# Kernel tuning notes

Hardware: AMD Instinct MI355X
Metric: run time of the kernel (lower is better)

Reference implementation:

```python
import jax, jax.numpy as jnp
import numpy as np

IN_DIM = 256
HID = 512
PAT = 10
B = 512
BN_EPS = 1e-5


def setup_inputs() -> dict:
    key = jax.random.key(0)
    ks = jax.random.split(key, 16)
    s = 0.05
    return {
        "x": jax.random.normal(ks[0], (B, IN_DIM), jnp.float32),
        # pattern_detector params
        "W1": jax.random.normal(ks[1], (HID, IN_DIM), jnp.float32) * s,
        "b1": jax.random.normal(ks[2], (HID,), jnp.float32) * s,
        "bn_gamma": 1.0 + jax.random.normal(ks[3], (HID,), jnp.float32) * s,
        "bn_beta": jax.random.normal(ks[4], (HID,), jnp.float32) * s,
        "bn_mean": jax.random.normal(ks[5], (HID,), jnp.float32) * s,
        "bn_var": jnp.ones((HID,), jnp.float32),
        "W2": jax.random.normal(ks[6], (HID // 2, HID), jnp.float32) * s,
        "b2": jax.random.normal(ks[7], (HID // 2,), jnp.float32) * s,
        "W3": jax.random.normal(ks[8], (PAT, HID // 2), jnp.float32) * s,
        "b3": jax.random.normal(ks[9], (PAT,), jnp.float32) * s,
        # similarity_layer params; first Linear weight [HID, 2*IN_DIM] split into
        # the half acting on x_i (Ws1_a) and the half acting on x_j (Ws1_b)
        "Ws1_a": jax.random.normal(ks[10], (HID, IN_DIM), jnp.float32) * s,
        "Ws1_b": jax.random.normal(ks[11], (HID, IN_DIM), jnp.float32) * s,
        "bs1": jax.random.normal(ks[12], (HID,), jnp.float32) * s,
        "ws2": jax.random.normal(ks[13], (HID,), jnp.float32) * s,
        "bs2": jax.random.normal(ks[14], (), jnp.float32) * s,
    }


def reference(x, W1, b1, bn_gamma, bn_beta, bn_mean, bn_var, W2, b2, W3, b3,
              Ws1_a, Ws1_b, bs1, ws2, bs2):
    # --- pattern_detector MLP (eval mode: BN uses running stats, dropout off) ---
    h = x @ W1.T + b1                                    # [B, HID]
    h = bn_gamma * (h - bn_mean) * jax.lax.rsqrt(bn_var + BN_EPS) + bn_beta
    h = jax.nn.relu(h)
    h2 = jax.nn.relu(h @ W2.T + b2)                      # [B, HID//2]
    pattern_scores = h2 @ W3.T + b3                      # [B, PAT]
    pattern_probs = jax.nn.softmax(pattern_scores, axis=-1)

    # --- pairwise similarity: sim(i,j) = MLP(concat(x_i, x_j)) ---
    # Linear([x_i; x_j]) = x_i @ Ws1_a^T + x_j @ Ws1_b^T + bs1, so precompute
    # the two GEMMs and broadcast-add instead of materializing [B,B,2*IN_DIM].
    A = x @ Ws1_a.T                                      # [B, HID]
    C = x @ Ws1_b.T                                      # [B, HID]
    hid = jax.nn.relu(A[:, None, :] + C[None, :, :] + bs1)  # [B, B, HID]
    logits = hid @ ws2 + bs2                             # [B, B]
    sim_full = jax.nn.sigmoid(logits)
    # Original loops i<j only and mirrors, diagonal stays 0. Results are
    # detached (.item()) in torch, so stop_gradient for faithfulness.
    iu = jnp.triu(jnp.ones((x.shape[0], x.shape[0]), sim_full.dtype), k=1)
    S = sim_full * iu
    similarities = jax.lax.stop_gradient(S + S.T)

    return pattern_probs, pattern_scores, similarities
```

## Files before the change

kernel.cpp:

```cpp
#include <hip/hip_runtime.h>
#include <math.h>

#define BN_EPS 1e-5f

typedef _Float16 half2v __attribute__((ext_vector_type(2)));
typedef _Float16 half4v __attribute__((ext_vector_type(4)));
typedef _Float16 half8v __attribute__((ext_vector_type(8)));
typedef __fp16 fp16x8 __attribute__((ext_vector_type(8)));
typedef float floatx4 __attribute__((ext_vector_type(4)));

__device__ __forceinline__ float fdot2(half2v a, half2v b, float c) {
    return __builtin_amdgcn_fdot2(a, b, c, false);
}
__device__ __forceinline__ half2v cvt2(float a, float b) {
    return __builtin_bit_cast(half2v, __builtin_amdgcn_cvt_pkrtz(a, b));
}
__device__ __forceinline__ floatx4 mfma16(half8v a, half8v b, floatx4 c) {
    return __builtin_amdgcn_mfma_f32_16x16x32_f16(
        __builtin_bit_cast(fp16x8, a), __builtin_bit_cast(fp16x8, b), c, 0, 0, 0);
}

__global__ __launch_bounds__(256) void fused3_mfma(
    const float* __restrict__ x,
    const float* __restrict__ W1, const float* __restrict__ b1,
    const float* __restrict__ g, const float* __restrict__ be,
    const float* __restrict__ mu, const float* __restrict__ va,
    const float* __restrict__ Wa, const float* __restrict__ bs1,
    const float* __restrict__ Wb,
    _Float16* __restrict__ h16, _Float16* __restrict__ A16,
    _Float16* __restrict__ C16)
{
    __shared__ _Float16 Xs[64][264];
    __shared__ _Float16 Ws[32][264];

    const int t  = threadIdx.x;
    const int n0 = blockIdx.x * 32;
    const int m0 = blockIdx.y * 64;
    const int z  = blockIdx.z;
    const float* __restrict__ Wp = (z == 0) ? W1 : (z == 1 ? Wa : Wb);

    #pragma unroll
    for (int i = 0; i < 16; ++i) {
        const int cidx = t + i * 256;
        const int row = cidx >> 6;
        const int c4  = cidx & 63;
        const float4 v = *(const float4*)&x[(m0 + row) * 256 + c4 * 4];
        *(half2v*)&Xs[row][c4 * 4 + 0] = cvt2(v.x, v.y);
        *(half2v*)&Xs[row][c4 * 4 + 2] = cvt2(v.z, v.w);
    }
    #pragma unroll
    for (int i = 0; i < 8; ++i) {
        const int cidx = t + i * 256;
        const int row = cidx >> 6;
        const int c4  = cidx & 63;
        const float4 v = *(const float4*)&Wp[(n0 + row) * 256 + c4 * 4];
        *(half2v*)&Ws[row][c4 * 4 + 0] = cvt2(v.x, v.y);
        *(half2v*)&Ws[row][c4 * 4 + 2] = cvt2(v.z, v.w);
    }
    __syncthreads();

    const int wave = t >> 6;
    const int lane = t & 63;
    const int wy = wave >> 1, wx = wave & 1;
    const int lrow = lane & 15;
    const int quad = lane >> 4;
    const int kq = quad * 8;

    floatx4 acc[2] = {{0.f, 0.f, 0.f, 0.f}, {0.f, 0.f, 0.f, 0.f}};

    #pragma unroll
    for (int kc = 0; kc < 256; kc += 32) {
        const half8v a0 = *(const half8v*)&Xs[wy * 32 + lrow][kc + kq];
        const half8v a1 = *(const half8v*)&Xs[wy * 32 + 16 + lrow][kc + kq];
        const half8v b0 = *(const half8v*)&Ws[wx * 16 + lrow][kc + kq];
        acc[0] = mfma16(a0, b0, acc[0]);
        acc[1] = mfma16(a1, b0, acc[1]);
    }

    const int n = n0 + wx * 16 + lrow;
    float scale, off;
    if (z == 0) {
        const float s = g[n] * rsqrtf(va[n] + BN_EPS);
        scale = s;
        off = (b1[n] - mu[n]) * s + be[n];
    } else if (z == 1) {
        scale = 1.f;
        off = bs1[n];
    } else {
        scale = 1.f;
        off = 0.f;
    }
    _Float16* __restrict__ dst = (z == 0) ? h16 : (z == 1 ? A16 : C16);
    #pragma unroll
    for (int mi = 0; mi < 2; ++mi) {
        #pragma unroll
        for (int r = 0; r < 4; ++r) {
            const int m = m0 + wy * 32 + mi * 16 + quad * 4 + r;
            float v = acc[mi][r] * scale + off;
            if (z == 0) v = fmaxf(v, 0.f);
            dst[m * 512 + n] = (_Float16)v;
        }
    }
}

__global__ __launch_bounds__(512) void gemm_h2_kernel(
    const _Float16* __restrict__ h16, const float* __restrict__ W2,
    const float* __restrict__ b2, float* __restrict__ h2o)
{
    __shared__ half2v As16[2][16][36];
    __shared__ half2v Bs16[2][16][72];
    __shared__ float Ps[32][68];

    const int t  = threadIdx.x;
    const int gk = t >> 8;
    const int tl = t & 255;
    const int m0 = blockIdx.y * 32;
    const int n0 = blockIdx.x * 64;
    const int tx = tl & 15, ty = tl >> 4;
    const int kb = gk << 8;

    float acc[2][4] = {};

    for (int kc = 0; kc < 256; kc += 32) {
        const int kk = kb + kc;
        if (tl < 128) {
            const int arow = tl >> 2;
            const int ak8  = (tl & 3) << 3;
            const float4 av = *(const float4*)&h16[(m0 + arow) * 512 + kk + ak8];
            const half2v* ap = (const half2v*)&av;
            const int k2 = ak8 >> 1;
            As16[gk][k2 + 0][arow] = ap[0];
            As16[gk][k2 + 1][arow] = ap[1];
            As16[gk][k2 + 2][arow] = ap[2];
            As16[gk][k2 + 3][arow] = ap[3];
        }
        {
            const int brow = tl >> 2;
            const int bk8  = (tl & 3) << 3;
            const float4 bv0 = *(const float4*)&W2[(n0 + brow) * 512 + kk + bk8];
            const float4 bv1 = *(const float4*)&W2[(n0 + brow) * 512 + kk + bk8 + 4];
            const int k2 = bk8 >> 1;
            Bs16[gk][k2 + 0][brow] = cvt2(bv0.x, bv0.y);
            Bs16[gk][k2 + 1][brow] = cvt2(bv0.z, bv0.w);
            Bs16[gk][k2 + 2][brow] = cvt2(bv1.x, bv1.y);
            Bs16[gk][k2 + 3][brow] = cvt2(bv1.z, bv1.w);
        }
        __syncthreads();

        #pragma unroll
        for (int k2 = 0; k2 < 16; ++k2) {
            const half4v a4 = *(const half4v*)&As16[gk][k2][ty * 2];
            const half8v b8 = *(const half8v*)&Bs16[gk][k2][tx * 4];
            const half2v a0 = __builtin_shufflevector(a4, a4, 0, 1);
            const half2v a1 = __builtin_shufflevector(a4, a4, 2, 3);
            const half2v b0 = __builtin_shufflevector(b8, b8, 0, 1);
            const half2v b1h = __builtin_shufflevector(b8, b8, 2, 3);
            const half2v b2h = __builtin_shufflevector(b8, b8, 4, 5);
            const half2v b3h = __builtin_shufflevector(b8, b8, 6, 7);
            acc[0][0] = fdot2(a0, b0, acc[0][0]);
            acc[0][1] = fdot2(a0, b1h, acc[0][1]);
            acc[0][2] = fdot2(a0, b2h, acc[0][2]);
            acc[0][3] = fdot2(a0, b3h, acc[0][3]);
            acc[1][0] = fdot2(a1, b0, acc[1][0]);
            acc[1][1] = fdot2(a1, b1h, acc[1][1]);
            acc[1][2] = fdot2(a1, b2h, acc[1][2]);
            acc[1][3] = fdot2(a1, b3h, acc[1][3]);
        }
        __syncthreads();
    }

    if (gk == 1) {
        #pragma unroll
        for (int i = 0; i < 2; ++i)
            #pragma unroll
            for (int j = 0; j < 4; ++j)
                Ps[ty * 2 + i][tx * 4 + j] = acc[i][j];
    }
    __syncthreads();
    if (gk == 0) {
        const int n = n0 + tx * 4;
        #pragma unroll
        for (int i = 0; i < 2; ++i) {
            const int m = m0 + ty * 2 + i;
            float4 o;
            o.x = fmaxf(acc[i][0] + Ps[ty * 2 + i][tx * 4 + 0] + b2[n + 0], 0.f);
            o.y = fmaxf(acc[i][1] + Ps[ty * 2 + i][tx * 4 + 1] + b2[n + 1], 0.f);
            o.z = fmaxf(acc[i][2] + Ps[ty * 2 + i][tx * 4 + 2] + b2[n + 2], 0.f);
            o.w = fmaxf(acc[i][3] + Ps[ty * 2 + i][tx * 4 + 3] + b2[n + 3], 0.f);
            *(float4*)&h2o[m * 256 + n] = o;
        }
    }
}

#define SIMS 260
__global__ __launch_bounds__(512) void tail_kernel(
    const float* __restrict__ h2, const float* __restrict__ W3,
    const float* __restrict__ b3,
    const _Float16* __restrict__ A16, const _Float16* __restrict__ C16,
    const float* __restrict__ ws2, const float* __restrict__ bs2,
    float* __restrict__ out)
{
    __shared__ _Float16 Rs[2][32][SIMS];
    __shared__ _Float16 Qs[2][32][SIMS];
    __shared__ half2v wsh[256];
    __shared__ float Ps[32][33];
    __shared__ float Tt[32][33];

    const int bid = blockIdx.x;
    const int t   = threadIdx.x;

    if (bid >= 256) {
        const int lane = t & 63;
        const int r = (bid - 256) * 8 + (t >> 6);

        float p[10];
        #pragma unroll
        for (int q = 0; q < 10; ++q) p[q] = 0.f;
        #pragma unroll
        for (int kk = 0; kk < 4; ++kk) {
            const int k = lane + kk * 64;
            const float hv = h2[r * 256 + k];
            #pragma unroll
            for (int q = 0; q < 10; ++q)
                p[q] = fmaf(hv, W3[q * 256 + k], p[q]);
        }
        #pragma unroll
        for (int q = 0; q < 10; ++q) {
            #pragma unroll
            for (int off = 32; off > 0; off >>= 1)
                p[q] += __shfl_down(p[q], off);
        }
        if (lane == 0) {
            float s[10], m = -1e30f;
            #pragma unroll
            for (int q = 0; q < 10; ++q) { s[q] = p[q] + b3[q]; m = fmaxf(m, s[q]); }
            float e[10], sum = 0.f;
            #pragma unroll
            for (int q = 0; q < 10; ++q) { e[q] = __expf(s[q] - m); sum += e[q]; }
            const float inv = 1.f / sum;
            #pragma unroll
            for (int q = 0; q < 10; ++q) {
                out[r * 10 + q] = e[q] * inv;
                out[5120 + r * 10 + q] = s[q];
            }
        }
        return;
    }

    float* __restrict__ S = out + 10240;
    const int gk = t >> 8;
    const int tl = t & 255;
    const int r0 = (bid >> 4) * 32;
    const int q0 = (bid & 15) * 32;
    const bool diag = (r0 == q0);
    const _Float16* RsSrc = (r0 <= q0) ? A16 : C16;
    const _Float16* QsSrc = (r0 <= q0) ? C16 : A16;
    const int kbase = gk << 8;

    if (t < 256) {
        half2v w;
        w.x = (_Float16)ws2[2 * t];
        w.y = (_Float16)ws2[2 * t + 1];
        wsh[t] = w;
    }

    #pragma unroll
    for (int i = 0; i < 4; ++i) {
        const int idx = tl + i * 256;
        const int row = idx >> 5;
        const int c8  = idx & 31;
        const float4 vr = *(const float4*)&RsSrc[(r0 + row) * 512 + kbase + c8 * 8];
        const float4 vq = *(const float4*)&QsSrc[(q0 + row) * 512 + kbase + c8 * 8];
        char* dr = (char*)&Rs[gk][row][0] + c8 * 16;
        ((float2*)dr)[0] = make_float2(vr.x, vr.y);
        ((float2*)dr)[1] = make_float2(vr.z, vr.w);
        char* dq = (char*)&Qs[gk][row][0] + c8 * 16;
        ((float2*)dq)[0] = make_float2(vq.x, vq.y);
        ((float2*)dq)[1] = make_float2(vq.z, vq.w);
    }
    __syncthreads();

    const int tx = tl & 15, ty = tl >> 4;
    const half2v* rp0 = (const half2v*)&Rs[gk][ty * 2][0];
    const half2v* rp1 = (const half2v*)&Rs[gk][ty * 2 + 1][0];
    const half2v* qp0 = (const half2v*)&Qs[gk][tx * 2][0];
    const half2v* qp1 = (const half2v*)&Qs[gk][tx * 2 + 1][0];
    const half2v* wp  = &wsh[gk * 128];
    const half2v z2 = {(_Float16)0, (_Float16)0};

    float a00 = 0.f, a01 = 0.f, a10 = 0.f, a11 = 0.f;
    #pragma unroll 16
    for (int k2 = 0; k2 < 128; ++k2) {
        const half2v r0v = rp0[k2], r1v = rp1[k2];
        const half2v q0v = qp0[k2], q1v = qp1[k2];
        const half2v w2 = wp[k2];
        a00 = fdot2(__builtin_elementwise_max(r0v + q0v, z2), w2, a00);
        a01 = fdot2(__builtin_elementwise_max(r0v + q1v, z2), w2, a01);
        a10 = fdot2(__builtin_elementwise_max(r1v + q0v, z2), w2, a10);
        a11 = fdot2(__builtin_elementwise_max(r1v + q1v, z2), w2, a11);
    }

    if (gk == 1) {
        Ps[ty * 2 + 0][tx * 2 + 0] = a00;
        Ps[ty * 2 + 0][tx * 2 + 1] = a01;
        Ps[ty * 2 + 1][tx * 2 + 0] = a10;
        Ps[ty * 2 + 1][tx * 2 + 1] = a11;
    }
    __syncthreads();

    if (gk == 0) {
        const float bsv = bs2[0];
        float v[2][2];
        v[0][0] = a00 + Ps[ty * 2 + 0][tx * 2 + 0];
        v[0][1] = a01 + Ps[ty * 2 + 0][tx * 2 + 1];
        v[1][0] = a10 + Ps[ty * 2 + 1][tx * 2 + 0];
        v[1][1] = a11 + Ps[ty * 2 + 1][tx * 2 + 1];
        #pragma unroll
        for (int di = 0; di < 2; ++di)
            #pragma unroll
            for (int dj = 0; dj < 2; ++dj)
                v[di][dj] = 1.f / (1.f + __expf(-(v[di][dj] + bsv)));
        if (!diag) {
            #pragma unroll
            for (int di = 0; di < 2; ++di)
                *(float2*)&S[(r0 + ty * 2 + di) * 512 + q0 + tx * 2] =
                    make_float2(v[di][0], v[di][1]);
        } else {
            #pragma unroll
            for (int di = 0; di < 2; ++di)
                #pragma unroll
                for (int dj = 0; dj < 2; ++dj)
                    Tt[ty * 2 + di][tx * 2 + dj] = v[di][dj];
        }
    }
    if (diag) {
        __syncthreads();
        if (gk == 0) {
            #pragma unroll
            for (int di = 0; di < 2; ++di)
                #pragma unroll
                for (int dj = 0; dj < 2; ++dj) {
                    const int rl = ty * 2 + di, ql = tx * 2 + dj;
                    const float o = rl < ql ? Tt[rl][ql] : (rl > ql ? Tt[ql][rl] : 0.f);
                    S[(r0 + rl) * 512 + q0 + ql] = o;
                }
        }
    }
}

extern "C" void kernel_launch(void* const* d_in, const int* in_sizes, int n_in,
                              void* d_out, int out_size, void* d_ws, size_t ws_size,
                              hipStream_t stream)
{
    const float* x   = (const float*)d_in[0];
    const float* W1  = (const float*)d_in[1];
    const float* b1  = (const float*)d_in[2];
    const float* g   = (const float*)d_in[3];
    const float* be  = (const float*)d_in[4];
    const float* mu  = (const float*)d_in[5];
    const float* va  = (const float*)d_in[6];
    const float* W2  = (const float*)d_in[7];
    const float* b2  = (const float*)d_in[8];
    const float* W3  = (const float*)d_in[9];
    const float* b3  = (const float*)d_in[10];
    const float* Wa  = (const float*)d_in[11];
    const float* Wb  = (const float*)d_in[12];
    const float* bs1 = (const float*)d_in[13];
    const float* ws2 = (const float*)d_in[14];
    const float* bs2 = (const float*)d_in[15];

    float* out = (float*)d_out;
    _Float16* h16 = (_Float16*)d_ws;
    float* h2 = (float*)(h16 + 512 * 512);
    _Float16* A16 = (_Float16*)(h2 + 512 * 256);
    _Float16* C16 = A16 + 512 * 512;

    fused3_mfma<<<dim3(16, 8, 3), 256, 0, stream>>>(x, W1, b1, g, be, mu, va,
                                                    Wa, bs1, Wb, h16, A16, C16);
    gemm_h2_kernel<<<dim3(4, 16), 512, 0, stream>>>(h16, W2, b2, h2);
    tail_kernel<<<320, 512, 0, stream>>>(h2, W3, b3, A16, C16, ws2, bs2, out);
}
```

Baseline: 111.0 us.

## Use MFMA for h2 GEMM and compute only upper-triangular similarity tiles

The fdot2-based h2 GEMM is replaced by a 16x16x32 MFMA kernel that stages full K rows in shared memory. The pairwise similarity kernel now launches only upper-triangular 16x16 tiles (528 blocks) and writes each result plus its mirrored transpose, avoiding the near-half of redundant lower-triangle work. It also drops the split-K reduction and uses one output per thread with smaller blocks. The trade-off is a serial per-thread loop over K=512 in the similarity tile and a small while-loop to decode the triangular tile index.

After: 101.3 us, median of 2. 1.1x faster.

```diff
diff --git a/kernel.cpp b/kernel.cpp
--- a/kernel.cpp
+++ b/kernel.cpp
@@ -4,7 +4,6 @@
 #define BN_EPS 1e-5f
 
 typedef _Float16 half2v __attribute__((ext_vector_type(2)));
-typedef _Float16 half4v __attribute__((ext_vector_type(4)));
 typedef _Float16 half8v __attribute__((ext_vector_type(8)));
 typedef __fp16 fp16x8 __attribute__((ext_vector_type(8)));
 typedef float floatx4 __attribute__((ext_vector_type(4)));
@@ -103,115 +102,81 @@
     }
 }
 
-__global__ __launch_bounds__(512) void gemm_h2_kernel(
+__global__ __launch_bounds__(256) void h2_mfma(
     const _Float16* __restrict__ h16, const float* __restrict__ W2,
     const float* __restrict__ b2, float* __restrict__ h2o)
 {
-    __shared__ half2v As16[2][16][36];
-    __shared__ half2v Bs16[2][16][72];
-    __shared__ float Ps[32][68];
+    __shared__ _Float16 Xs[32][520];
+    __shared__ _Float16 Ws[32][520];
 
     const int t  = threadIdx.x;
-    const int gk = t >> 8;
-    const int tl = t & 255;
+    const int n0 = blockIdx.x * 32;
     const int m0 = blockIdx.y * 32;
-    const int n0 = blockIdx.x * 64;
-    const int tx = tl & 15, ty = tl >> 4;
-    const int kb = gk << 8;
-
-    float acc[2][4] = {};
-
-    for (int kc = 0; kc < 256; kc += 32) {
-        const int kk = kb + kc;
-        if (tl < 128) {
-            const int arow = tl >> 2;
-            const int ak8  = (tl & 3) << 3;
-            const float4 av = *(const float4*)&h16[(m0 + arow) * 512 + kk + ak8];
-            const half2v* ap = (const half2v*)&av;
-            const int k2 = ak8 >> 1;
-            As16[gk][k2 + 0][arow] = ap[0];
-            As16[gk][k2 + 1][arow] = ap[1];
-            As16[gk][k2 + 2][arow] = ap[2];
-            As16[gk][k2 + 3][arow] = ap[3];
-        }
-        {
-            const int brow = tl >> 2;
-            const int bk8  = (tl & 3) << 3;
-            const float4 bv0 = *(const float4*)&W2[(n0 + brow) * 512 + kk + bk8];
-            const float4 bv1 = *(const float4*)&W2[(n0 + brow) * 512 + kk + bk8 + 4];
-            const int k2 = bk8 >> 1;
-            Bs16[gk][k2 + 0][brow] = cvt2(bv0.x, bv0.y);
-            Bs16[gk][k2 + 1][brow] = cvt2(bv0.z, bv0.w);
-            Bs16[gk][k2 + 2][brow] = cvt2(bv1.x, bv1.y);
-            Bs16[gk][k2 + 3][brow] = cvt2(bv1.z, bv1.w);
-        }
-        __syncthreads();
-
-        #pragma unroll
-        for (int k2 = 0; k2 < 16; ++k2) {
-            const half4v a4 = *(const half4v*)&As16[gk][k2][ty * 2];
-            const half8v b8 = *(const half8v*)&Bs16[gk][k2][tx * 4];
-            const half2v a0 = __builtin_shufflevector(a4, a4, 0, 1);
-            const half2v a1 = __builtin_shufflevector(a4, a4, 2, 3);
-            const half2v b0 = __builtin_shufflevector(b8, b8, 0, 1);
-            const half2v b1h = __builtin_shufflevector(b8, b8, 2, 3);
-            const half2v b2h = __builtin_shufflevector(b8, b8, 4, 5);
-            const half2v b3h = __builtin_shufflevector(b8, b8, 6, 7);
-            acc[0][0] = fdot2(a0, b0, acc[0][0]);
-            acc[0][1] = fdot2(a0, b1h, acc[0][1]);
-            acc[0][2] = fdot2(a0, b2h, acc[0][2]);
-            acc[0][3] = fdot2(a0, b3h, acc[0][3]);
-            acc[1][0] = fdot2(a1, b0, acc[1][0]);
-            acc[1][1] = fdot2(a1, b1h, acc[1][1]);
-            acc[1][2] = fdot2(a1, b2h, acc[1][2]);
-            acc[1][3] = fdot2(a1, b3h, acc[1][3]);
-        }
-        __syncthreads();
-    }
-
-    if (gk == 1) {
-        #pragma unroll
-        for (int i = 0; i < 2; ++i)
-            #pragma unroll
-            for (int j = 0; j < 4; ++j)
-                Ps[ty * 2 + i][tx * 4 + j] = acc[i][j];
-    }
-    __syncthreads();
-    if (gk == 0) {
-        const int n = n0 + tx * 4;
-        #pragma unroll
-        for (int i = 0; i < 2; ++i) {
-            const int m = m0 + ty * 2 + i;
-            float4 o;
-            o.x = fmaxf(acc[i][0] + Ps[ty * 2 + i][tx * 4 + 0] + b2[n + 0], 0.f);
-            o.y = fmaxf(acc[i][1] + Ps[ty * 2 + i][tx * 4 + 1] + b2[n + 1], 0.f);
-            o.z = fmaxf(acc[i][2] + Ps[ty * 2 + i][tx * 4 + 2] + b2[n + 2], 0.f);
-            o.w = fmaxf(acc[i][3] + Ps[ty * 2 + i][tx * 4 + 3] + b2[n + 3], 0.f);
-            *(float4*)&h2o[m * 256 + n] = o;
-        }
-    }
-}
-
-#define SIMS 260
-__global__ __launch_bounds__(512) void tail_kernel(
+
+    #pragma unroll
+    for (int i = 0; i < 8; ++i) {
+        const int cidx = t + i * 256;
+        const int row = cidx >> 6;
+        const int c8  = cidx & 63;
+        const float4 v = *(const float4*)&h16[(m0 + row) * 512 + c8 * 8];
+        *(half8v*)&Xs[row][c8 * 8] = __builtin_bit_cast(half8v, v);
+    }
+    #pragma unroll
+    for (int i = 0; i < 8; ++i) {
+        const int cidx = t + i * 256;
+        const int row = cidx >> 6;
+        const int c8  = cidx & 63;
+        const float4 v0 = *(const float4*)&W2[(n0 + row) * 512 + c8 * 8];
+        const float4 v1 = *(const float4*)&W2[(n0 + row) * 512 + c8 * 8 + 4];
+        *(half2v*)&Ws[row][c8 * 8 + 0] = cvt2(v0.x, v0.y);
+        *(half2v*)&Ws[row][c8 * 8 + 2] = cvt2(v0.z, v0.w);
+        *(half2v*)&Ws[row][c8 * 8 + 4] = cvt2(v1.x, v1.y);
+        *(half2v*)&Ws[row][c8 * 8 + 6] = cvt2(v1.z, v1.w);
+    }
+    __syncthreads();
+
+    const int wave = t >> 6;
+    const int lane = t & 63;
+    const int wy = wave >> 1, wx = wave & 1;
+    const int lrow = lane & 15;
+    const int quad = lane >> 4;
+    const int kq = quad * 8;
+
+    floatx4 acc = {0.f, 0.f, 0.f, 0.f};
+    #pragma unroll
+    for (int kc = 0; kc < 512; kc += 32) {
+        const half8v a = *(const half8v*)&Xs[wy * 16 + lrow][kc + kq];
+        const half8v b = *(const half8v*)&Ws[wx * 16 + lrow][kc + kq];
+        acc = mfma16(a, b, acc);
+    }
+
+    const int n = n0 + wx * 16 + lrow;
+    const float bb = b2[n];
+    #pragma unroll
+    for (int r = 0; r < 4; ++r) {
+        const int m = m0 + wy * 16 + quad * 4 + r;
+        h2o[m * 256 + n] = fmaxf(acc[r] + bb, 0.f);
+    }
+}
+
+__global__ __launch_bounds__(256) void tail_kernel(
     const float* __restrict__ h2, const float* __restrict__ W3,
     const float* __restrict__ b3,
     const _Float16* __restrict__ A16, const _Float16* __restrict__ C16,
     const float* __restrict__ ws2, const float* __restrict__ bs2,
     float* __restrict__ out)
 {
-    __shared__ _Float16 Rs[2][32][SIMS];
-    __shared__ _Float16 Qs[2][32][SIMS];
+    __shared__ _Float16 Rs[16][520];
+    __shared__ _Float16 Qs[16][520];
     __shared__ half2v wsh[256];
-    __shared__ float Ps[32][33];
-    __shared__ float Tt[32][33];
+    __shared__ float Tt[16][17];
 
     const int bid = blockIdx.x;
     const int t   = threadIdx.x;
 
-    if (bid >= 256) {
+    if (bid >= 528) {
         const int lane = t & 63;
-        const int r = (bid - 256) * 8 + (t >> 6);
+        const int r = (bid - 528) * 4 + (t >> 6);
 
         float p[10];
         #pragma unroll
@@ -248,103 +213,55 @@
     }
 
     float* __restrict__ S = out + 10240;
-    const int gk = t >> 8;
-    const int tl = t & 255;
-    const int r0 = (bid >> 4) * 32;
-    const int q0 = (bid & 15) * 32;
-    const bool diag = (r0 == q0);
-    const _Float16* RsSrc = (r0 <= q0) ? A16 : C16;
-    const _Float16* QsSrc = (r0 <= q0) ? C16 : A16;
-    const int kbase = gk << 8;
-
-    if (t < 256) {
+    int jt = 0;
+    {
+        int b = bid;
+        while ((jt + 1) * (jt + 2) / 2 <= b) ++jt;
+    }
+    const int it = bid - jt * (jt + 1) / 2;
+    const int r0 = it * 16, q0 = jt * 16;
+    const bool diag = (it == jt);
+
+    {
         half2v w;
         w.x = (_Float16)ws2[2 * t];
         w.y = (_Float16)ws2[2 * t + 1];
         wsh[t] = w;
     }
-
     #pragma unroll
     for (int i = 0; i < 4; ++i) {
-        const int idx = tl + i * 256;
-        const int row = idx >> 5;
-        const int c8  = idx & 31;
-        const float4 vr = *(const float4*)&RsSrc[(r0 + row) * 512 + kbase + c8 * 8];
-        const float4 vq = *(const float4*)&QsSrc[(q0 + row) * 512 + kbase + c8 * 8];
-        char* dr = (char*)&Rs[gk][row][0] + c8 * 16;
-        ((float2*)dr)[0] = make_float2(vr.x, vr.y);
-        ((float2*)dr)[1] = make_float2(vr.z, vr.w);
-        char* dq = (char*)&Qs[gk][row][0] + c8 * 16;
-        ((float2*)dq)[0] = make_float2(vq.x, vq.y);
-        ((float2*)dq)[1] = make_float2(vq.z, vq.w);
-    }
-    __syncthreads();
-
-    const int tx = tl & 15, ty = tl >> 4;
-    const half2v* rp0 = (const half2v*)&Rs[gk][ty * 2][0];
-    const half2v* rp1 = (const half2v*)&Rs[gk][ty * 2 + 1][0];
-    const half2v* qp0 = (const half2v*)&Qs[gk][tx * 2][0];
-    const half2v* qp1 = (const half2v*)&Qs[gk][tx * 2 + 1][0];
-    const half2v* wp  = &wsh[gk * 128];
+        const int cidx = t + i * 256;
+        const int row = cidx >> 6;
+        const int c8  = cidx & 63;
+        const float4 vr = *(const float4*)&A16[(r0 + row) * 512 + c8 * 8];
+        const float4 vq = *(const float4*)&C16[(q0 + row) * 512 + c8 * 8];
+        *(half8v*)&Rs[row][c8 * 8] = __builtin_bit_cast(half8v, vr);
+        *(half8v*)&Qs[row][c8 * 8] = __builtin_bit_cast(half8v, vq);
+    }
+    __syncthreads();
+
+    const int tx = t & 15, ty = t >> 4;
+    const half2v* rp = (const half2v*)&Rs[ty][0];
+    const half2v* qp = (const half2v*)&Qs[tx][0];
     const half2v z2 = {(_Float16)0, (_Float16)0};
 
-    float a00 = 0.f, a01 = 0.f, a10 = 0.f, a11 = 0.f;
-    #pragma unroll 16
-    for (int k2 = 0; k2 < 128; ++k2) {
-        const half2v r0v = rp0[k2], r1v = rp1[k2];
-        const half2v q0v = qp0[k2], q1v = qp1[k2];
-        const half2v w2 = wp[k2];
-        a00 = fdot2(__builtin_elementwise_max(r0v + q0v, z2), w2, a00);
-        a01 = fdot2(__builtin_elementwise_max(r0v + q1v, z2), w2, a01);
-        a10 = fdot2(__builtin_elementwise_max(r1v + q0v, z2), w2, a10);
-        a11 = fdot2(__builtin_elementwise_max(r1v + q1v, z2), w2, a11);
-    }
-
-    if (gk == 1) {
-        Ps[ty * 2 + 0][tx * 2 + 0] = a00;
-        Ps[ty * 2 + 0][tx * 2 + 1] = a01;
-        Ps[ty * 2 + 1][tx * 2 + 0] = a10;
-        Ps[ty * 2 + 1][tx * 2 + 1] = a11;
-    }
-    __syncthreads();
-
-    if (gk == 0) {
-        const float bsv = bs2[0];
-        float v[2][2];
-        v[0][0] = a00 + Ps[ty * 2 + 0][tx * 2 + 0];
-        v[0][1] = a01 + Ps[ty * 2 + 0][tx * 2 + 1];
-        v[1][0] = a10 + Ps[ty * 2 + 1][tx * 2 + 0];
-        v[1][1] = a11 + Ps[ty * 2 + 1][tx * 2 + 1];
-        #pragma unroll
-        for (int di = 0; di < 2; ++di)
-            #pragma unroll
-            for (int dj = 0; dj < 2; ++dj)
-                v[di][dj] = 1.f / (1.f + __expf(-(v[di][dj] + bsv)));
-        if (!diag) {
-            #pragma unroll
-            for (int di = 0; di < 2; ++di)
-                *(float2*)&S[(r0 + ty * 2 + di) * 512 + q0 + tx * 2] =
-                    make_float2(v[di][0], v[di][1]);
-        } else {
-            #pragma unroll
-            for (int di = 0; di < 2; ++di)
-                #pragma unroll
-                for (int dj = 0; dj < 2; ++dj)
-                    Tt[ty * 2 + di][tx * 2 + dj] = v[di][dj];
-        }
-    }
+    float a0 = 0.f;
+    #pragma unroll 8
+    for (int k2 = 0; k2 < 256; ++k2) {
+        a0 = fdot2(__builtin_elementwise_max(rp[k2] + qp[k2], z2), wsh[k2], a0);
+    }
+    const float v = 1.f / (1.f + __expf(-(a0 + bs2[0])));
+
+    Tt[ty][tx] = v;
+    __syncthreads();
+
     if (diag) {
-        __syncthreads();
-        if (gk == 0) {
-            #pragma unroll
-            for (int di = 0; di < 2; ++di)
-                #pragma unroll
-                for (int dj = 0; dj < 2; ++dj) {
-                    const int rl = ty * 2 + di, ql = tx * 2 + dj;
-                    const float o = rl < ql ? Tt[rl][ql] : (rl > ql ? Tt[ql][rl] : 0.f);
-                    S[(r0 + rl) * 512 + q0 + ql] = o;
-                }
-        }
+        const int r = r0 + ty, q = q0 + tx;
+        const float o = (r < q) ? Tt[ty][tx] : (r > q ? Tt[tx][ty] : 0.f);
+        S[r * 512 + q] = o;
+    } else {
+        S[(r0 + ty) * 512 + q0 + tx] = v;
+        S[(q0 + ty) * 512 + r0 + tx] = Tt[tx][ty];
     }
 }
 
@@ -377,6 +294,6 @@
 
     fused3_mfma<<<dim3(16, 8, 3), 256, 0, stream>>>(x, W1, b1, g, be, mu, va,
                                                     Wa, bs1, Wb, h16, A16, C16);
-    gemm_h2_kernel<<<dim3(4, 16), 512, 0, stream>>>(h16, W2, b2, h2);
-    tail_kernel<<<320, 512, 0, stream>>>(h2, W3, b3, A16, C16, ws2, bs2, out);
-}
+    h2_mfma<<<dim3(8, 16), 256, 0, stream>>>(h16, W2, b2, h2);
+    tail_kernel<<<656, 256, 0, stream>>>(h2, W3, b3, A16, C16, ws2, bs2, out);
+}
```
